# Performance work log

Measured on AMD Instinct MI355X. Metric: run time of the kernel, lower is better.

Reference implementation:

```python
import jax, jax.numpy as jnp
import numpy as np

HEADS = 4
GROUPS = 32
EPS = 1e-5


def setup_inputs() -> dict:
    key = jax.random.key(0)
    ks = jax.random.split(key, 3)
    B, C, H, W = 8, 256, 32, 32
    x = jax.random.normal(ks[0], (B, C, H, W), dtype=jnp.float32)
    gamma = jnp.ones((C,), jnp.float32)
    beta = jnp.zeros((C,), jnp.float32)
    w_qkv = jax.random.normal(ks[1], (3 * C, C), jnp.float32) * (1.0 / np.sqrt(C))
    b_qkv = jnp.zeros((3 * C,), jnp.float32)
    w_proj = jax.random.normal(ks[2], (C, C), jnp.float32) * (1.0 / np.sqrt(C))
    b_proj = jnp.zeros((C,), jnp.float32)
    return {"x": x, "gamma": gamma, "beta": beta, "w_qkv": w_qkv,
            "b_qkv": b_qkv, "w_proj": w_proj, "b_proj": b_proj}


def group_norm(x, gamma, beta):
    B, C, H, W = x.shape
    xg = x.reshape(B, GROUPS, C // GROUPS, H, W)
    mean = xg.mean(axis=(2, 3, 4), keepdims=True)
    var = xg.var(axis=(2, 3, 4), keepdims=True)
    xg = (xg - mean) * jax.lax.rsqrt(var + EPS)
    xn = xg.reshape(B, C, H, W)
    return xn * gamma[None, :, None, None] + beta[None, :, None, None]


def reference(x, gamma, beta, w_qkv, b_qkv, w_proj, b_proj):
    B, C, H, W = x.shape
    hd = C // HEADS  # head dim
    h = group_norm(x, gamma, beta)
    # 1x1 conv == channel matmul: [B,3C,H,W]
    qkv = jnp.einsum('oc,bchw->bohw', w_qkv, h) + b_qkv[None, :, None, None]
    qkv = qkv.reshape(B, 3, HEADS, hd, H * W)
    q, k, v = qkv[:, 0], qkv[:, 1], qkv[:, 2]  # each [B, heads, hd, HW]
    attn = jnp.einsum('bhci,bhcj->bhij', q, k) * (hd ** -0.5)
    attn = jax.nn.softmax(attn, axis=-1)
    out = jnp.einsum('bhij,bhcj->bhci', attn, v).reshape(B, C, H, W)
    proj = jnp.einsum('oc,bchw->bohw', w_proj, out) + b_proj[None, :, None, None]
    return x + proj
```

## Files before the change

kernel.cpp:

```cpp
#include <hip/hip_runtime.h>
#include <hip/hip_bf16.h>

static constexpr int kC = 256;
static constexpr int kN = 1024;

using s16x8 = __attribute__((ext_vector_type(8))) short;
using f32x4 = __attribute__((ext_vector_type(4))) float;
using u32x4 = __attribute__((ext_vector_type(4))) unsigned int;

__device__ inline f32x4 mfma16(s16x8 a, s16x8 b, f32x4 c) {
  return __builtin_amdgcn_mfma_f32_16x16x32_bf16(a, b, c, 0, 0, 0);
}

__device__ inline unsigned short f2bf(float f) {
  unsigned u = __builtin_bit_cast(unsigned, f);
  u = (u + 0x7fffu + ((u >> 16) & 1u)) >> 16;
  return (unsigned short)u;
}

__device__ inline float exp2_fast(float x) {
  float r;
  asm("v_exp_f32 %0, %1" : "=v"(r) : "v"(x));
  return r;
}

__device__ inline unsigned cvt_pk_bf16(float lo, float hi) {
  unsigned r;
  asm("v_cvt_pk_bf16_f32 %0, %1, %2" : "=v"(r) : "v"(lo), "v"(hi));
  return r;
}

static constexpr float kQScale = 0.18033688011112042f;

__global__ __launch_bounds__(256) void prep_kernel(
    const float* __restrict__ x, const float* __restrict__ gamma,
    const float* __restrict__ beta, unsigned short* __restrict__ hTp,
    const float* __restrict__ wq, const float* __restrict__ wp,
    unsigned short* __restrict__ Wqp, unsigned short* __restrict__ Wpp) {
  if (blockIdx.x < 128) {
    const int tid = blockIdx.x * 256 + threadIdx.x;
    const float* src;
    unsigned short* dst;
    if (tid < 24576) {
      const int fragid = tid >> 6, lane = tid & 63;
      const int Mt = fragid >> 3, kt = fragid & 7;
      src = wq + (size_t)(Mt * 16 + (lane & 15)) * 256 + kt * 32 + (lane >> 4) * 8;
      dst = Wqp + (size_t)tid * 8;
    } else {
      const int id = tid - 24576;
      const int fragid = id >> 6, lane = id & 63;
      const int Mt = fragid >> 3, kt = fragid & 7;
      src = wp + (size_t)(Mt * 16 + (lane & 15)) * 256 + kt * 32 + (lane >> 4) * 8;
      dst = Wpp + (size_t)id * 8;
    }
    const float4 f0 = *(const float4*)src;
    const float4 f1 = *(const float4*)(src + 4);
    ushort4 o0, o1;
    o0.x = f2bf(f0.x); o0.y = f2bf(f0.y); o0.z = f2bf(f0.z); o0.w = f2bf(f0.w);
    o1.x = f2bf(f1.x); o1.y = f2bf(f1.y); o1.z = f2bf(f1.z); o1.w = f2bf(f1.w);
    *(ushort4*)dst = o0;
    *(ushort4*)(dst + 4) = o1;
    return;
  }

  const int bg = blockIdx.x - 128;
  const int b = bg & 7, g = bg >> 3;
  const size_t base = ((size_t)b * kC + (size_t)g * 8) * kN;
  const float4* __restrict__ x4 = (const float4*)(x + base);
  const int t = threadIdx.x;

  float vv[8][4];
  float s = 0.f, ss = 0.f;
#pragma unroll
  for (int i = 0; i < 8; ++i) {
    const float4 v = x4[t + 256 * i];
    vv[i][0] = v.x; vv[i][1] = v.y; vv[i][2] = v.z; vv[i][3] = v.w;
    s += v.x + v.y + v.z + v.w;
    ss += v.x * v.x + v.y * v.y + v.z * v.z + v.w * v.w;
  }
#pragma unroll
  for (int off = 32; off > 0; off >>= 1) {
    s += __shfl_xor(s, off);
    ss += __shfl_xor(ss, off);
  }
  __shared__ float rs[4], rss[4];
  const int wave = t >> 6, lane = t & 63;
  if (lane == 0) { rs[wave] = s; rss[wave] = ss; }
  __syncthreads();
  s = rs[0] + rs[1] + rs[2] + rs[3];
  ss = rss[0] + rss[1] + rss[2] + rss[3];
  const float mean = s * (1.f / 8192.f);
  const float var = ss * (1.f / 8192.f) - mean * mean;
  const float rinv = rsqrtf(var + 1e-5f);
  float ga[8], be[8];
#pragma unroll
  for (int i = 0; i < 8; ++i) {
    ga[i] = gamma[g * 8 + i] * rinv;
    be[i] = beta[g * 8 + i] - mean * ga[i];
  }
  const int kt = g >> 2, gq = g & 3;
#pragma unroll
  for (int r = 0; r < 4; ++r) {
    const int pos = 4 * t + r;
    const int nt = pos >> 4, lp = pos & 15;
    unsigned short* dst =
        hTp + ((size_t)((b * 64 + nt) * 8 + kt) * 64 + (gq * 16 + lp)) * 8;
    ushort4 o0, o1;
    o0.x = f2bf(vv[0][r] * ga[0] + be[0]);
    o0.y = f2bf(vv[1][r] * ga[1] + be[1]);
    o0.z = f2bf(vv[2][r] * ga[2] + be[2]);
    o0.w = f2bf(vv[3][r] * ga[3] + be[3]);
    o1.x = f2bf(vv[4][r] * ga[4] + be[4]);
    o1.y = f2bf(vv[5][r] * ga[5] + be[5]);
    o1.z = f2bf(vv[6][r] * ga[6] + be[6]);
    o1.w = f2bf(vv[7][r] * ga[7] + be[7]);
    *(ushort4*)dst = o0;
    *(ushort4*)(dst + 4) = o1;
  }
}

__device__ inline void gload(const s16x8* __restrict__ Af,
                             const s16x8* __restrict__ Bf,
                             int Mt0, int Nt0, int kt, int lane,
                             s16x8 (&a)[4], s16x8 (&bb)[2]) {
#pragma unroll
  for (int mt = 0; mt < 4; ++mt)
    a[mt] = Af[((size_t)(Mt0 + mt) * 8 + kt) * 64 + lane];
#pragma unroll
  for (int nt = 0; nt < 2; ++nt)
    bb[nt] = Bf[((size_t)(Nt0 + nt) * 8 + kt) * 64 + lane];
}

__device__ inline void gmfma(const s16x8 (&a)[4], const s16x8 (&bb)[2],
                             f32x4 (&acc)[4][2], bool swap) {
  if (swap) {
#pragma unroll
    for (int mt = 0; mt < 4; ++mt)
#pragma unroll
      for (int nt = 0; nt < 2; ++nt)
        acc[mt][nt] = mfma16(bb[nt], a[mt], acc[mt][nt]);
  } else {
#pragma unroll
    for (int mt = 0; mt < 4; ++mt)
#pragma unroll
      for (int nt = 0; nt < 2; ++nt)
        acc[mt][nt] = mfma16(a[mt], bb[nt], acc[mt][nt]);
  }
}

__global__ __launch_bounds__(256) void gemm_qkv_kernel(
    const unsigned short* __restrict__ Wp, const float* __restrict__ bias,
    const unsigned short* __restrict__ Bp,
    unsigned short* __restrict__ Qp, unsigned short* __restrict__ Kp,
    unsigned short* __restrict__ Vp) {
  const int bid = blockIdx.x;
  const int swz = (bid & 7) * 96 + (bid >> 3);
  const int b = swz / 96, rr = swz % 96;
  const int mb = rr >> 4, nb = rr & 15;
  const int t = threadIdx.x;
  const int wave = t >> 6, lane = t & 63;
  const int li = lane & 15, grp = lane >> 4;
  const int m0 = mb * 128 + (wave >> 1) * 64;
  const int n0 = nb * 64 + (wave & 1) * 32;
  const bool swap = mb >= 4;
  const int Mt0 = m0 >> 4;
  const int Nt0 = b * 64 + (n0 >> 4);
  const s16x8* __restrict__ Af = (const s16x8*)Wp;
  const s16x8* __restrict__ Bf = (const s16x8*)Bp;

  f32x4 acc[4][2];
#pragma unroll
  for (int mt = 0; mt < 4; ++mt)
#pragma unroll
    for (int nt = 0; nt < 2; ++nt) acc[mt][nt] = f32x4{0.f, 0.f, 0.f, 0.f};

  s16x8 sa[4][4], sb[4][2];
  gload(Af, Bf, Mt0, Nt0, 0, lane, sa[0], sb[0]);
  gload(Af, Bf, Mt0, Nt0, 1, lane, sa[1], sb[1]);
  gload(Af, Bf, Mt0, Nt0, 2, lane, sa[2], sb[2]);
#pragma unroll
  for (int kt = 0; kt < 8; ++kt) {
    if (kt + 3 < 8)
      gload(Af, Bf, Mt0, Nt0, kt + 3, lane, sa[(kt + 3) & 3], sb[(kt + 3) & 3]);
    gmfma(sa[kt & 3], sb[kt & 3], acc, swap);
  }

  if (!swap) {
    unsigned short* __restrict__ Tp = (mb < 2) ? Qp : Kp;
    const float qs = (mb < 2) ? kQScale : 1.0f;
#pragma unroll
    for (int mt = 0; mt < 4; ++mt) {
      const int mbase = m0 + mt * 16;
      const int head = (mbase >> 6) & 3;
      const int bh = b * 4 + head;
      const int c16 = mbase & 63;
      const int ks = c16 >> 5;
      const int grpp = ((c16 >> 3) + (grp >> 1)) & 3;
      const float4 bv = *(const float4*)(bias + mbase + 4 * grp);
#pragma unroll
      for (int nt = 0; nt < 2; ++nt) {
        const int pt = (n0 >> 4) + nt;
        ushort4 o;
        o.x = f2bf((acc[mt][nt][0] + bv.x) * qs);
        o.y = f2bf((acc[mt][nt][1] + bv.y) * qs);
        o.z = f2bf((acc[mt][nt][2] + bv.z) * qs);
        o.w = f2bf((acc[mt][nt][3] + bv.w) * qs);
        *(ushort4*)(Tp + (size_t)bh * 65536 +
                    ((size_t)(pt * 2 + ks) * 64 + grpp * 16 + li) * 8 +
                    (grp & 1) * 4) = o;
      }
    }
  } else {
#pragma unroll
    for (int mt = 0; mt < 4; ++mt) {
      const int mbase = m0 + mt * 16;
      const int head = (mbase >> 6) & 3;
      const int bh = b * 4 + head;
      const int ct = (mbase & 63) >> 4;
      const float bvc = bias[mbase + li];
      const int kvt = n0 >> 5;
#pragma unroll
      for (int nt = 0; nt < 2; ++nt) {
        ushort4 o;
        o.x = f2bf(acc[mt][nt][0] + bvc);
        o.y = f2bf(acc[mt][nt][1] + bvc);
        o.z = f2bf(acc[mt][nt][2] + bvc);
        o.w = f2bf(acc[mt][nt][3] + bvc);
        *(ushort4*)(Vp + (size_t)bh * 65536 +
                    ((size_t)(ct * 32 + kvt) * 64 + grp * 16 + li) * 8 +
                    nt * 4) = o;
      }
    }
  }
}

__global__ __launch_bounds__(512) void attn_proj_kernel(
    const unsigned short* __restrict__ Qp, const unsigned short* __restrict__ Kp,
    const unsigned short* __restrict__ Vp, const unsigned short* __restrict__ Wpp,
    const float* __restrict__ bpj, const float* __restrict__ x,
    float* __restrict__ out) {
  __shared__ __align__(16) unsigned short Ex[2][8][64][8];
  const int bid = blockIdx.x;
  const int swz = (bid & 7) * 32 + (bid >> 3);
  const int b = swz >> 5, qb = swz & 31;
  const int t = threadIdx.x;
  const int w8 = t >> 6, lane = t & 63;
  const int head = w8 & 3, qh = w8 >> 2;
  const int li = lane & 15, grp = lane >> 4;
  const int q0 = qb * 32 + qh * 16;
  const int bh = b * 4 + head;
  const unsigned short* __restrict__ Qb = Qp + (size_t)bh * 65536;
  const unsigned short* __restrict__ Kb = Kp + (size_t)bh * 65536;
  const unsigned short* __restrict__ Vb = Vp + (size_t)bh * 65536;

  s16x8 qf[2];
#pragma unroll
  for (int ks = 0; ks < 2; ++ks)
    qf[ks] = *(const s16x8*)(Qb + (((q0 >> 4) * 2 + ks) * 64 + lane) * 8);

  f32x4 O[4];
#pragma unroll
  for (int ct = 0; ct < 4; ++ct) O[ct] = f32x4{0.f, 0.f, 0.f, 0.f};
  f32x4 lvec = f32x4{0.f, 0.f, 0.f, 0.f};
  float m_run = -1.0e30f;

  auto loadK = [&](int it, s16x8 (&kk)[2][2]) {
#pragma unroll
    for (int mt = 0; mt < 2; ++mt)
#pragma unroll
      for (int ks = 0; ks < 2; ++ks)
        kk[mt][ks] = *(const s16x8*)(
            Kb + ((size_t)((it * 2 + mt) * 2 + ks) * 64 + lane) * 8);
  };
  auto loadV = [&](int it, s16x8 (&vv)[4]) {
#pragma unroll
    for (int ct = 0; ct < 4; ++ct)
      vv[ct] = *(const s16x8*)(Vb + ((size_t)(ct * 32 + it) * 64 + lane) * 8);
  };
  auto qkt = [&](const s16x8 (&kk)[2][2], f32x4 (&s)[2]) {
    __builtin_amdgcn_s_setprio(1);
#pragma unroll
    for (int mt = 0; mt < 2; ++mt) {
      s[mt] = mfma16(kk[mt][0], qf[0], f32x4{0.f, 0.f, 0.f, 0.f});
      s[mt] = mfma16(kk[mt][1], qf[1], s[mt]);
    }
    __builtin_amdgcn_s_setprio(0);
  };
  auto smaxpv = [&](f32x4 (&s)[2], const s16x8 (&vv)[4]) {
    const float A = fmaxf(fmaxf(s[0][0], s[0][1]), s[0][2]);
    const float B = fmaxf(fmaxf(s[0][3], s[1][0]), s[1][1]);
    const float C = fmaxf(fmaxf(s[1][2], s[1][3]), A);
    float pm = fmaxf(B, C);
    pm = fmaxf(pm, __shfl_xor(pm, 16));
    pm = fmaxf(pm, __shfl_xor(pm, 32));
    if (!__all(pm <= m_run + 8.0f)) {
      const float mnew = fmaxf(m_run, pm);
      const float f = exp2_fast(m_run - mnew);
      m_run = mnew;
      lvec *= f;
#pragma unroll
      for (int ct = 0; ct < 4; ++ct) O[ct] *= f;
    }
    f32x4 p[2];
#pragma unroll
    for (int mt = 0; mt < 2; ++mt) {
#pragma unroll
      for (int r = 0; r < 4; ++r) p[mt][r] = exp2_fast(s[mt][r] - m_run);
      lvec += p[mt];
    }
    u32x4 pk;
    pk[0] = cvt_pk_bf16(p[0][0], p[0][1]);
    pk[1] = cvt_pk_bf16(p[0][2], p[0][3]);
    pk[2] = cvt_pk_bf16(p[1][0], p[1][1]);
    pk[3] = cvt_pk_bf16(p[1][2], p[1][3]);
    const s16x8 pf = __builtin_bit_cast(s16x8, pk);
    __builtin_amdgcn_s_setprio(1);
#pragma unroll
    for (int ct = 0; ct < 4; ++ct) O[ct] = mfma16(vv[ct], pf, O[ct]);
    __builtin_amdgcn_s_setprio(0);
  };

  s16x8 K4[4][2][2], V4[4][4];
  loadK(0, K4[0]); loadK(1, K4[1]); loadK(2, K4[2]); loadK(3, K4[3]);
  loadV(0, V4[0]); loadV(1, V4[1]); loadV(2, V4[2]); loadV(3, V4[3]);
  f32x4 sc[2];
  qkt(K4[0], sc);
  loadK(4, K4[0]);

#pragma unroll 1
  for (int g = 0; g < 8; ++g) {
    const int t0 = g * 4;
#pragma unroll
    for (int j = 0; j < 4; ++j) {
      const int tt = t0 + j;
      f32x4 sn[2];
      qkt(K4[(j + 1) & 3], sn);
      loadK(tt + 5, K4[(j + 1) & 3]);
      smaxpv(sc, V4[j]);
      loadV(tt + 4, V4[j]);
      sc[0] = sn[0];
      sc[1] = sn[1];
    }
  }

  float lt = lvec[0] + lvec[1] + lvec[2] + lvec[3];
  lt += __shfl_xor(lt, 16);
  lt += __shfl_xor(lt, 32);
  const float rinv = 1.f / lt;
#pragma unroll
  for (int ct = 0; ct < 4; ++ct) {
    const int ktp = head * 2 + (ct >> 1);
    const int grpp = ((ct & 1) * 2 + (grp >> 1)) & 3;
    ushort4 o;
    o.x = f2bf(O[ct][0] * rinv);
    o.y = f2bf(O[ct][1] * rinv);
    o.z = f2bf(O[ct][2] * rinv);
    o.w = f2bf(O[ct][3] * rinv);
    *(ushort4*)&Ex[qh][ktp][grpp * 16 + li][(grp & 1) * 4] = o;
  }
  __syncthreads();

  {
    const int Mt0 = w8 * 2;
    const s16x8* __restrict__ Af = (const s16x8*)Wpp;
    f32x4 acc[2][2];
#pragma unroll
    for (int mt = 0; mt < 2; ++mt)
#pragma unroll
      for (int nt = 0; nt < 2; ++nt) acc[mt][nt] = f32x4{0.f, 0.f, 0.f, 0.f};

    s16x8 pa[3][2];
    auto loadA = [&](int kt, s16x8 (&a)[2]) {
#pragma unroll
      for (int mt = 0; mt < 2; ++mt)
        a[mt] = Af[((size_t)(Mt0 + mt) * 8 + kt) * 64 + lane];
    };
    loadA(0, pa[0]);
    loadA(1, pa[1]);
#pragma unroll
    for (int kt = 0; kt < 8; ++kt) {
      if (kt + 2 < 8) loadA(kt + 2, pa[(kt + 2) % 3]);
      s16x8 bb[2];
#pragma unroll
      for (int nt = 0; nt < 2; ++nt)
        bb[nt] = *(const s16x8*)&Ex[nt][kt][lane][0];
#pragma unroll
      for (int mt = 0; mt < 2; ++mt)
#pragma unroll
        for (int nt = 0; nt < 2; ++nt)
          acc[mt][nt] = mfma16(pa[kt % 3][mt], bb[nt], acc[mt][nt]);
    }

#pragma unroll
    for (int mt = 0; mt < 2; ++mt) {
      const int mbase = w8 * 32 + mt * 16 + 4 * grp;
      const float4 bv = *(const float4*)(bpj + mbase);
      const float bvr[4] = {bv.x, bv.y, bv.z, bv.w};
#pragma unroll
      for (int nt = 0; nt < 2; ++nt) {
        const int pos = qb * 32 + nt * 16 + li;
#pragma unroll
        for (int r2 = 0; r2 < 4; ++r2) {
          const size_t ob = ((size_t)(b * 256 + mbase + r2)) * 1024 + pos;
          out[ob] = acc[mt][nt][r2] + bvr[r2] + x[ob];
        }
      }
    }
  }
}

extern "C" void kernel_launch(void* const* d_in, const int* in_sizes, int n_in,
                              void* d_out, int out_size, void* d_ws, size_t ws_size,
                              hipStream_t stream) {
  const float* x      = (const float*)d_in[0];
  const float* gamma  = (const float*)d_in[1];
  const float* beta   = (const float*)d_in[2];
  const float* w_qkv  = (const float*)d_in[3];
  const float* b_qkv  = (const float*)d_in[4];
  const float* w_proj = (const float*)d_in[5];
  const float* b_proj = (const float*)d_in[6];
  float* out = (float*)d_out;

  unsigned short* ws = (unsigned short*)d_ws;
  unsigned short* Wqp  = ws;
  unsigned short* Wpp  = Wqp + 196608;
  unsigned short* hTp  = Wpp + 65536;
  unsigned short* Qp   = hTp + 2097152;
  unsigned short* Kp   = Qp + 2097152;
  unsigned short* Vp   = Kp + 2097152;

  hipLaunchKernelGGL(prep_kernel, dim3(384), dim3(256), 0, stream,
                     x, gamma, beta, hTp, w_qkv, w_proj, Wqp, Wpp);
  hipLaunchKernelGGL(gemm_qkv_kernel, dim3(768), dim3(256), 0, stream,
                     Wqp, b_qkv, hTp, Qp, Kp, Vp);
  hipLaunchKernelGGL(attn_proj_kernel, dim3(256), dim3(512), 0, stream,
                     Qp, Kp, Vp, Wpp, b_proj, x, out);
}
```

Measured before the change: 42.58 us.

## Split attention and projection, stage K/V tiles in LDS shared across query waves

The fused attention+projection kernel is split into two kernels. In the new attention kernel, each 256-thread block handles one (batch, head) with 64 queries over four waves. K/V tiles are loaded once per block into double-buffered LDS with global_load_lds and shared by all waves, instead of every wave streaming its own register copies. The output projection becomes a separate GEMM kernel that reads attention output from a new workspace buffer. This adds a kernel launch, a global round trip for the attention output, and a per-iteration __syncthreads that replaces the deep register prefetch pipeline.

Measured after the change: 51.06 us. +19.9%, slower.

```diff
diff --git a/kernel.cpp b/kernel.cpp
--- a/kernel.cpp
+++ b/kernel.cpp
@@ -28,6 +28,12 @@
   unsigned r;
   asm("v_cvt_pk_bf16_f32 %0, %1, %2" : "=v"(r) : "v"(lo), "v"(hi));
   return r;
+}
+
+__device__ inline void gl_lds16(const void* g, void* l) {
+  typedef __attribute__((address_space(1))) const unsigned int GU;
+  typedef __attribute__((address_space(3))) unsigned int LU;
+  __builtin_amdgcn_global_load_lds((GU*)g, (LU*)l, 16, 0, 0);
 }
 
 static constexpr float kQScale = 0.18033688011112042f;
@@ -234,21 +240,20 @@
   }
 }
 
-__global__ __launch_bounds__(512) void attn_proj_kernel(
+__global__ __launch_bounds__(256) void attn_kernel(
     const unsigned short* __restrict__ Qp, const unsigned short* __restrict__ Kp,
-    const unsigned short* __restrict__ Vp, const unsigned short* __restrict__ Wpp,
-    const float* __restrict__ bpj, const float* __restrict__ x,
-    float* __restrict__ out) {
-  __shared__ __align__(16) unsigned short Ex[2][8][64][8];
+    const unsigned short* __restrict__ Vp, unsigned short* __restrict__ aoTp) {
+  __shared__ __align__(16) unsigned short Kl[2][2048];
+  __shared__ __align__(16) unsigned short Vl[2][2048];
   const int bid = blockIdx.x;
-  const int swz = (bid & 7) * 32 + (bid >> 3);
-  const int b = swz >> 5, qb = swz & 31;
+  const int xcd = bid & 7, idx = bid >> 3;
+  const int bh = xcd * 4 + (idx & 3);
+  const int qb = idx >> 2;
+  const int b = bh >> 2, head = bh & 3;
   const int t = threadIdx.x;
-  const int w8 = t >> 6, lane = t & 63;
-  const int head = w8 & 3, qh = w8 >> 2;
+  const int wave = t >> 6, lane = t & 63;
   const int li = lane & 15, grp = lane >> 4;
-  const int q0 = qb * 32 + qh * 16;
-  const int bh = b * 4 + head;
+  const int q0 = qb * 64 + wave * 16;
   const unsigned short* __restrict__ Qb = Qp + (size_t)bh * 65536;
   const unsigned short* __restrict__ Kb = Kp + (size_t)bh * 65536;
   const unsigned short* __restrict__ Vb = Vp + (size_t)bh * 65536;
@@ -264,20 +269,27 @@
   f32x4 lvec = f32x4{0.f, 0.f, 0.f, 0.f};
   float m_run = -1.0e30f;
 
-  auto loadK = [&](int it, s16x8 (&kk)[2][2]) {
+  auto stage = [&](int it, int nb) {
+    const unsigned short* ksrc = Kb + ((size_t)(it * 4 + wave) * 512 + lane * 8);
+    gl_lds16(ksrc, &Kl[nb][wave * 512]);
+    const unsigned short* vsrc = Vb + ((size_t)(wave * 32 + it) * 512 + lane * 8);
+    gl_lds16(vsrc, &Vl[nb][wave * 512]);
+  };
+
+  stage(0, 0);
+  __syncthreads();
+
+  int cb = 0;
+#pragma unroll 1
+  for (int it = 0; it < 32; ++it) {
+    if (it < 31) stage(it + 1, cb ^ 1);
+    s16x8 kk[2][2];
 #pragma unroll
     for (int mt = 0; mt < 2; ++mt)
 #pragma unroll
       for (int ks = 0; ks < 2; ++ks)
-        kk[mt][ks] = *(const s16x8*)(
-            Kb + ((size_t)((it * 2 + mt) * 2 + ks) * 64 + lane) * 8);
-  };
-  auto loadV = [&](int it, s16x8 (&vv)[4]) {
-#pragma unroll
-    for (int ct = 0; ct < 4; ++ct)
-      vv[ct] = *(const s16x8*)(Vb + ((size_t)(ct * 32 + it) * 64 + lane) * 8);
-  };
-  auto qkt = [&](const s16x8 (&kk)[2][2], f32x4 (&s)[2]) {
+        kk[mt][ks] = *(const s16x8*)&Kl[cb][(mt * 2 + ks) * 512 + lane * 8];
+    f32x4 s[2];
     __builtin_amdgcn_s_setprio(1);
 #pragma unroll
     for (int mt = 0; mt < 2; ++mt) {
@@ -285,8 +297,6 @@
       s[mt] = mfma16(kk[mt][1], qf[1], s[mt]);
     }
     __builtin_amdgcn_s_setprio(0);
-  };
-  auto smaxpv = [&](f32x4 (&s)[2], const s16x8 (&vv)[4]) {
     const float A = fmaxf(fmaxf(s[0][0], s[0][1]), s[0][2]);
     const float B = fmaxf(fmaxf(s[0][3], s[1][0]), s[1][1]);
     const float C = fmaxf(fmaxf(s[1][2], s[1][3]), A);
@@ -314,33 +324,16 @@
     pk[2] = cvt_pk_bf16(p[1][0], p[1][1]);
     pk[3] = cvt_pk_bf16(p[1][2], p[1][3]);
     const s16x8 pf = __builtin_bit_cast(s16x8, pk);
+    s16x8 vv[4];
+#pragma unroll
+    for (int ct = 0; ct < 4; ++ct)
+      vv[ct] = *(const s16x8*)&Vl[cb][ct * 512 + lane * 8];
     __builtin_amdgcn_s_setprio(1);
 #pragma unroll
     for (int ct = 0; ct < 4; ++ct) O[ct] = mfma16(vv[ct], pf, O[ct]);
     __builtin_amdgcn_s_setprio(0);
-  };
-
-  s16x8 K4[4][2][2], V4[4][4];
-  loadK(0, K4[0]); loadK(1, K4[1]); loadK(2, K4[2]); loadK(3, K4[3]);
-  loadV(0, V4[0]); loadV(1, V4[1]); loadV(2, V4[2]); loadV(3, V4[3]);
-  f32x4 sc[2];
-  qkt(K4[0], sc);
-  loadK(4, K4[0]);
-
-#pragma unroll 1
-  for (int g = 0; g < 8; ++g) {
-    const int t0 = g * 4;
-#pragma unroll
-    for (int j = 0; j < 4; ++j) {
-      const int tt = t0 + j;
-      f32x4 sn[2];
-      qkt(K4[(j + 1) & 3], sn);
-      loadK(tt + 5, K4[(j + 1) & 3]);
-      smaxpv(sc, V4[j]);
-      loadV(tt + 4, V4[j]);
-      sc[0] = sn[0];
-      sc[1] = sn[1];
-    }
+    __syncthreads();
+    cb ^= 1;
   }
 
   float lt = lvec[0] + lvec[1] + lvec[2] + lvec[3];
@@ -356,54 +349,59 @@
     o.y = f2bf(O[ct][1] * rinv);
     o.z = f2bf(O[ct][2] * rinv);
     o.w = f2bf(O[ct][3] * rinv);
-    *(ushort4*)&Ex[qh][ktp][grpp * 16 + li][(grp & 1) * 4] = o;
-  }
-  __syncthreads();
-
-  {
-    const int Mt0 = w8 * 2;
-    const s16x8* __restrict__ Af = (const s16x8*)Wpp;
-    f32x4 acc[2][2];
-#pragma unroll
-    for (int mt = 0; mt < 2; ++mt)
-#pragma unroll
-      for (int nt = 0; nt < 2; ++nt) acc[mt][nt] = f32x4{0.f, 0.f, 0.f, 0.f};
-
-    s16x8 pa[3][2];
-    auto loadA = [&](int kt, s16x8 (&a)[2]) {
-#pragma unroll
-      for (int mt = 0; mt < 2; ++mt)
-        a[mt] = Af[((size_t)(Mt0 + mt) * 8 + kt) * 64 + lane];
-    };
-    loadA(0, pa[0]);
-    loadA(1, pa[1]);
-#pragma unroll
-    for (int kt = 0; kt < 8; ++kt) {
-      if (kt + 2 < 8) loadA(kt + 2, pa[(kt + 2) % 3]);
-      s16x8 bb[2];
-#pragma unroll
-      for (int nt = 0; nt < 2; ++nt)
-        bb[nt] = *(const s16x8*)&Ex[nt][kt][lane][0];
-#pragma unroll
-      for (int mt = 0; mt < 2; ++mt)
-#pragma unroll
-        for (int nt = 0; nt < 2; ++nt)
-          acc[mt][nt] = mfma16(pa[kt % 3][mt], bb[nt], acc[mt][nt]);
-    }
-
-#pragma unroll
-    for (int mt = 0; mt < 2; ++mt) {
-      const int mbase = w8 * 32 + mt * 16 + 4 * grp;
-      const float4 bv = *(const float4*)(bpj + mbase);
-      const float bvr[4] = {bv.x, bv.y, bv.z, bv.w};
-#pragma unroll
-      for (int nt = 0; nt < 2; ++nt) {
-        const int pos = qb * 32 + nt * 16 + li;
-#pragma unroll
-        for (int r2 = 0; r2 < 4; ++r2) {
-          const size_t ob = ((size_t)(b * 256 + mbase + r2)) * 1024 + pos;
-          out[ob] = acc[mt][nt][r2] + bvr[r2] + x[ob];
-        }
+    *(ushort4*)(aoTp +
+                ((size_t)((b * 64 + (q0 >> 4)) * 8 + ktp) * 64 + grpp * 16 + li) * 8 +
+                (grp & 1) * 4) = o;
+  }
+}
+
+__global__ __launch_bounds__(256) void gemm_proj_kernel(
+    const unsigned short* __restrict__ Wpp, const float* __restrict__ bias,
+    const unsigned short* __restrict__ aoTp, const float* __restrict__ res,
+    float* __restrict__ outp) {
+  const int bid = blockIdx.x;
+  const int swz = (bid & 7) * 32 + (bid >> 3);
+  const int b = swz >> 5, rr = swz & 31;
+  const int mb = rr >> 4, nb = rr & 15;
+  const int t = threadIdx.x;
+  const int wave = t >> 6, lane = t & 63;
+  const int li = lane & 15, grp = lane >> 4;
+  const int m0 = mb * 128 + (wave >> 1) * 64;
+  const int n0 = nb * 64 + (wave & 1) * 32;
+  const int Mt0 = m0 >> 4;
+  const int Nt0 = b * 64 + (n0 >> 4);
+  const s16x8* __restrict__ Af = (const s16x8*)Wpp;
+  const s16x8* __restrict__ Bf = (const s16x8*)aoTp;
+
+  f32x4 acc[4][2];
+#pragma unroll
+  for (int mt = 0; mt < 4; ++mt)
+#pragma unroll
+    for (int nt = 0; nt < 2; ++nt) acc[mt][nt] = f32x4{0.f, 0.f, 0.f, 0.f};
+
+  s16x8 sa[4][4], sb[4][2];
+  gload(Af, Bf, Mt0, Nt0, 0, lane, sa[0], sb[0]);
+  gload(Af, Bf, Mt0, Nt0, 1, lane, sa[1], sb[1]);
+  gload(Af, Bf, Mt0, Nt0, 2, lane, sa[2], sb[2]);
+#pragma unroll
+  for (int kt = 0; kt < 8; ++kt) {
+    if (kt + 3 < 8)
+      gload(Af, Bf, Mt0, Nt0, kt + 3, lane, sa[(kt + 3) & 3], sb[(kt + 3) & 3]);
+    gmfma(sa[kt & 3], sb[kt & 3], acc, false);
+  }
+
+#pragma unroll
+  for (int mt = 0; mt < 4; ++mt) {
+    const int mbase = m0 + mt * 16 + 4 * grp;
+    const float4 bv = *(const float4*)(bias + mbase);
+    const float bvr[4] = {bv.x, bv.y, bv.z, bv.w};
+#pragma unroll
+    for (int nt = 0; nt < 2; ++nt) {
+      const int pos = n0 + nt * 16 + li;
+#pragma unroll
+      for (int r = 0; r < 4; ++r) {
+        const size_t ob = ((size_t)(b * 256 + mbase + r)) * 1024 + pos;
+        outp[ob] = acc[mt][nt][r] + bvr[r] + res[ob];
       }
     }
   }
@@ -428,11 +426,14 @@
   unsigned short* Qp   = hTp + 2097152;
   unsigned short* Kp   = Qp + 2097152;
   unsigned short* Vp   = Kp + 2097152;
+  unsigned short* aoTp = Vp + 2097152;
 
   hipLaunchKernelGGL(prep_kernel, dim3(384), dim3(256), 0, stream,
                      x, gamma, beta, hTp, w_qkv, w_proj, Wqp, Wpp);
   hipLaunchKernelGGL(gemm_qkv_kernel, dim3(768), dim3(256), 0, stream,
                      Wqp, b_qkv, hTp, Qp, Kp, Vp);
-  hipLaunchKernelGGL(attn_proj_kernel, dim3(256), dim3(512), 0, stream,
-                     Qp, Kp, Vp, Wpp, b_proj, x, out);
-}
+  hipLaunchKernelGGL(attn_kernel, dim3(512), dim3(256), 0, stream,
+                     Qp, Kp, Vp, aoTp);
+  hipLaunchKernelGGL(gemm_proj_kernel, dim3(256), dim3(256), 0, stream,
+                     Wpp, b_proj, aoTp, x, out);
+}
```

## Split attention keys across waves and merge partial softmax states in LDS

Applied to the files above, without the earlier changes.

The attention kernel now gives each block 16 query positions instead of 32 and doubles the grid to 512 blocks. The two wave halves each process half of the key sequence, and the partial O, max and sum are combined through shared memory, split-K flash-decoding style. The deep register prefetch ring for K/V is dropped in favour of a simple loop with launch_bounds occupancy hint 4, aiming for more parallelism and occupancy on 256 CUs. The risks are the loss of explicit load/compute overlap, an extra LDS merge and sync, and half the reuse of the projection weights per block.

Measured after the change: 42.48 us. Within noise of the previous version (-0.2%).

```diff
diff --git a/kernel.cpp b/kernel.cpp
--- a/kernel.cpp
+++ b/kernel.cpp
@@ -234,20 +234,21 @@
   }
 }
 
-__global__ __launch_bounds__(512) void attn_proj_kernel(
+__global__ __launch_bounds__(512, 4) void attn_proj_kernel(
     const unsigned short* __restrict__ Qp, const unsigned short* __restrict__ Kp,
     const unsigned short* __restrict__ Vp, const unsigned short* __restrict__ Wpp,
     const float* __restrict__ bpj, const float* __restrict__ x,
     float* __restrict__ out) {
-  __shared__ __align__(16) unsigned short Ex[2][8][64][8];
+  __shared__ __align__(16) float Ml[4][64][18];
+  __shared__ __align__(16) unsigned short Ex[8][64][8];
   const int bid = blockIdx.x;
-  const int swz = (bid & 7) * 32 + (bid >> 3);
-  const int b = swz >> 5, qb = swz & 31;
+  const int b = bid & 7;
+  const int pb = bid >> 3;
+  const int q0 = pb * 16;
   const int t = threadIdx.x;
   const int w8 = t >> 6, lane = t & 63;
-  const int head = w8 & 3, qh = w8 >> 2;
+  const int head = w8 & 3, khalf = w8 >> 2;
   const int li = lane & 15, grp = lane >> 4;
-  const int q0 = qb * 32 + qh * 16;
   const int bh = b * 4 + head;
   const unsigned short* __restrict__ Qb = Qp + (size_t)bh * 65536;
   const unsigned short* __restrict__ Kb = Kp + (size_t)bh * 65536;
@@ -256,28 +257,30 @@
   s16x8 qf[2];
 #pragma unroll
   for (int ks = 0; ks < 2; ++ks)
-    qf[ks] = *(const s16x8*)(Qb + (((q0 >> 4) * 2 + ks) * 64 + lane) * 8);
+    qf[ks] = *(const s16x8*)(Qb + ((pb * 2 + ks) * 64 + lane) * 8);
 
   f32x4 O[4];
 #pragma unroll
   for (int ct = 0; ct < 4; ++ct) O[ct] = f32x4{0.f, 0.f, 0.f, 0.f};
   f32x4 lvec = f32x4{0.f, 0.f, 0.f, 0.f};
   float m_run = -1.0e30f;
-
-  auto loadK = [&](int it, s16x8 (&kk)[2][2]) {
+  const int kbase = khalf * 16;
+
+#pragma unroll 1
+  for (int i2 = 0; i2 < 16; ++i2) {
+    const int it = kbase + i2;
+    s16x8 kk[2][2];
 #pragma unroll
     for (int mt = 0; mt < 2; ++mt)
 #pragma unroll
       for (int ks = 0; ks < 2; ++ks)
         kk[mt][ks] = *(const s16x8*)(
             Kb + ((size_t)((it * 2 + mt) * 2 + ks) * 64 + lane) * 8);
-  };
-  auto loadV = [&](int it, s16x8 (&vv)[4]) {
+    s16x8 vv[4];
 #pragma unroll
     for (int ct = 0; ct < 4; ++ct)
       vv[ct] = *(const s16x8*)(Vb + ((size_t)(ct * 32 + it) * 64 + lane) * 8);
-  };
-  auto qkt = [&](const s16x8 (&kk)[2][2], f32x4 (&s)[2]) {
+    f32x4 s[2];
     __builtin_amdgcn_s_setprio(1);
 #pragma unroll
     for (int mt = 0; mt < 2; ++mt) {
@@ -285,8 +288,6 @@
       s[mt] = mfma16(kk[mt][1], qf[1], s[mt]);
     }
     __builtin_amdgcn_s_setprio(0);
-  };
-  auto smaxpv = [&](f32x4 (&s)[2], const s16x8 (&vv)[4]) {
     const float A = fmaxf(fmaxf(s[0][0], s[0][1]), s[0][2]);
     const float B = fmaxf(fmaxf(s[0][3], s[1][0]), s[1][1]);
     const float C = fmaxf(fmaxf(s[1][2], s[1][3]), A);
@@ -318,56 +319,49 @@
 #pragma unroll
     for (int ct = 0; ct < 4; ++ct) O[ct] = mfma16(vv[ct], pf, O[ct]);
     __builtin_amdgcn_s_setprio(0);
-  };
-
-  s16x8 K4[4][2][2], V4[4][4];
-  loadK(0, K4[0]); loadK(1, K4[1]); loadK(2, K4[2]); loadK(3, K4[3]);
-  loadV(0, V4[0]); loadV(1, V4[1]); loadV(2, V4[2]); loadV(3, V4[3]);
-  f32x4 sc[2];
-  qkt(K4[0], sc);
-  loadK(4, K4[0]);
-
-#pragma unroll 1
-  for (int g = 0; g < 8; ++g) {
-    const int t0 = g * 4;
-#pragma unroll
-    for (int j = 0; j < 4; ++j) {
-      const int tt = t0 + j;
-      f32x4 sn[2];
-      qkt(K4[(j + 1) & 3], sn);
-      loadK(tt + 5, K4[(j + 1) & 3]);
-      smaxpv(sc, V4[j]);
-      loadV(tt + 4, V4[j]);
-      sc[0] = sn[0];
-      sc[1] = sn[1];
-    }
   }
 
   float lt = lvec[0] + lvec[1] + lvec[2] + lvec[3];
   lt += __shfl_xor(lt, 16);
   lt += __shfl_xor(lt, 32);
-  const float rinv = 1.f / lt;
-#pragma unroll
-  for (int ct = 0; ct < 4; ++ct) {
-    const int ktp = head * 2 + (ct >> 1);
-    const int grpp = ((ct & 1) * 2 + (grp >> 1)) & 3;
-    ushort4 o;
-    o.x = f2bf(O[ct][0] * rinv);
-    o.y = f2bf(O[ct][1] * rinv);
-    o.z = f2bf(O[ct][2] * rinv);
-    o.w = f2bf(O[ct][3] * rinv);
-    *(ushort4*)&Ex[qh][ktp][grpp * 16 + li][(grp & 1) * 4] = o;
+
+  if (khalf == 1) {
+    float* dst = &Ml[head][lane][0];
+#pragma unroll
+    for (int ct = 0; ct < 4; ++ct) *(f32x4*)(dst + ct * 4) = O[ct];
+    dst[16] = m_run;
+    dst[17] = lt;
+  }
+  __syncthreads();
+  if (khalf == 0) {
+    const float* src = &Ml[head][lane][0];
+    const float mB = src[16], lB = src[17];
+    const float mS = fmaxf(m_run, mB);
+    const float fA = exp2_fast(m_run - mS);
+    const float fB = exp2_fast(mB - mS);
+    const float rinv = 1.f / (lt * fA + lB * fB);
+    const float a = fA * rinv, bs = fB * rinv;
+#pragma unroll
+    for (int ct = 0; ct < 4; ++ct) {
+      const f32x4 ob = *(const f32x4*)(src + ct * 4);
+      ushort4 o;
+      o.x = f2bf(O[ct][0] * a + ob[0] * bs);
+      o.y = f2bf(O[ct][1] * a + ob[1] * bs);
+      o.z = f2bf(O[ct][2] * a + ob[2] * bs);
+      o.w = f2bf(O[ct][3] * a + ob[3] * bs);
+      const int ktp = head * 2 + (ct >> 1);
+      const int grpp = ((ct & 1) * 2 + (grp >> 1)) & 3;
+      *(ushort4*)&Ex[ktp][grpp * 16 + li][(grp & 1) * 4] = o;
+    }
   }
   __syncthreads();
 
   {
     const int Mt0 = w8 * 2;
     const s16x8* __restrict__ Af = (const s16x8*)Wpp;
-    f32x4 acc[2][2];
-#pragma unroll
-    for (int mt = 0; mt < 2; ++mt)
-#pragma unroll
-      for (int nt = 0; nt < 2; ++nt) acc[mt][nt] = f32x4{0.f, 0.f, 0.f, 0.f};
+    f32x4 acc[2];
+    acc[0] = f32x4{0.f, 0.f, 0.f, 0.f};
+    acc[1] = f32x4{0.f, 0.f, 0.f, 0.f};
 
     s16x8 pa[3][2];
     auto loadA = [&](int kt, s16x8 (&a)[2]) {
@@ -380,15 +374,10 @@
 #pragma unroll
     for (int kt = 0; kt < 8; ++kt) {
       if (kt + 2 < 8) loadA(kt + 2, pa[(kt + 2) % 3]);
-      s16x8 bb[2];
-#pragma unroll
-      for (int nt = 0; nt < 2; ++nt)
-        bb[nt] = *(const s16x8*)&Ex[nt][kt][lane][0];
+      const s16x8 bb = *(const s16x8*)&Ex[kt][lane][0];
 #pragma unroll
       for (int mt = 0; mt < 2; ++mt)
-#pragma unroll
-        for (int nt = 0; nt < 2; ++nt)
-          acc[mt][nt] = mfma16(pa[kt % 3][mt], bb[nt], acc[mt][nt]);
+        acc[mt] = mfma16(pa[kt % 3][mt], bb, acc[mt]);
     }
 
 #pragma unroll
@@ -396,14 +385,11 @@
       const int mbase = w8 * 32 + mt * 16 + 4 * grp;
       const float4 bv = *(const float4*)(bpj + mbase);
       const float bvr[4] = {bv.x, bv.y, bv.z, bv.w};
-#pragma unroll
-      for (int nt = 0; nt < 2; ++nt) {
-        const int pos = qb * 32 + nt * 16 + li;
-#pragma unroll
-        for (int r2 = 0; r2 < 4; ++r2) {
-          const size_t ob = ((size_t)(b * 256 + mbase + r2)) * 1024 + pos;
-          out[ob] = acc[mt][nt][r2] + bvr[r2] + x[ob];
-        }
+      const int pos = q0 + li;
+#pragma unroll
+      for (int r2 = 0; r2 < 4; ++r2) {
+        const size_t ob = ((size_t)(b * 256 + mbase + r2)) * 1024 + pos;
+        out[ob] = acc[mt][r2] + bvr[r2] + x[ob];
       }
     }
   }
@@ -433,6 +419,6 @@
                      x, gamma, beta, hTp, w_qkv, w_proj, Wqp, Wpp);
   hipLaunchKernelGGL(gemm_qkv_kernel, dim3(768), dim3(256), 0, stream,
                      Wqp, b_qkv, hTp, Qp, Kp, Vp);
-  hipLaunchKernelGGL(attn_proj_kernel, dim3(256), dim3(512), 0, stream,
+  hipLaunchKernelGGL(attn_proj_kernel, dim3(512), dim3(512), 0, stream,
                      Qp, Kp, Vp, Wpp, b_proj, x, out);
 }
```

## Split KV range across wave pairs with split-K softmax merge in LDS

Applied to the files above, without the earlier changes.

Each wave now handles both 16-query halves of a 32-query block for one head, but only half of the key/value sequence. Partial outputs, running max and sum are merged through shared memory before the projection stage. This halves K/V loads per wave, because each loaded K/V tile serves two query tiles, and shortens the serial loop. In exchange it adds a merge step, an extra barrier and about 37KB more shared memory. The block-to-batch mapping and swizzle also change, and the deep four-stage prefetch is replaced by double buffering.

Result: faster. 36.06 us, median of 2 (-15.3%).

```diff
diff --git a/kernel.cpp b/kernel.cpp
--- a/kernel.cpp
+++ b/kernel.cpp
@@ -239,30 +239,37 @@
     const unsigned short* __restrict__ Vp, const unsigned short* __restrict__ Wpp,
     const float* __restrict__ bpj, const float* __restrict__ x,
     float* __restrict__ out) {
+  __shared__ __align__(16) float Ml[4][2][64][18];
   __shared__ __align__(16) unsigned short Ex[2][8][64][8];
   const int bid = blockIdx.x;
-  const int swz = (bid & 7) * 32 + (bid >> 3);
-  const int b = swz >> 5, qb = swz & 31;
+  const int b = bid & 7;
+  const int pb = bid >> 3;
   const int t = threadIdx.x;
   const int w8 = t >> 6, lane = t & 63;
-  const int head = w8 & 3, qh = w8 >> 2;
+  const int head = w8 & 3, khalf = w8 >> 2;
   const int li = lane & 15, grp = lane >> 4;
-  const int q0 = qb * 32 + qh * 16;
   const int bh = b * 4 + head;
   const unsigned short* __restrict__ Qb = Qp + (size_t)bh * 65536;
   const unsigned short* __restrict__ Kb = Kp + (size_t)bh * 65536;
   const unsigned short* __restrict__ Vb = Vp + (size_t)bh * 65536;
 
-  s16x8 qf[2];
-#pragma unroll
-  for (int ks = 0; ks < 2; ++ks)
-    qf[ks] = *(const s16x8*)(Qb + (((q0 >> 4) * 2 + ks) * 64 + lane) * 8);
-
-  f32x4 O[4];
-#pragma unroll
-  for (int ct = 0; ct < 4; ++ct) O[ct] = f32x4{0.f, 0.f, 0.f, 0.f};
-  f32x4 lvec = f32x4{0.f, 0.f, 0.f, 0.f};
-  float m_run = -1.0e30f;
+  s16x8 qf[2][2];
+#pragma unroll
+  for (int qh = 0; qh < 2; ++qh)
+#pragma unroll
+    for (int ks = 0; ks < 2; ++ks)
+      qf[qh][ks] = *(const s16x8*)(Qb + (((pb * 2 + qh) * 2 + ks) * 64 + lane) * 8);
+
+  f32x4 O[2][4];
+  f32x4 lvec[2];
+  float m_run[2] = {-1.0e30f, -1.0e30f};
+#pragma unroll
+  for (int qh = 0; qh < 2; ++qh) {
+    lvec[qh] = f32x4{0.f, 0.f, 0.f, 0.f};
+#pragma unroll
+    for (int ct = 0; ct < 4; ++ct) O[qh][ct] = f32x4{0.f, 0.f, 0.f, 0.f};
+  }
+  const int kbase = khalf * 16;
 
   auto loadK = [&](int it, s16x8 (&kk)[2][2]) {
 #pragma unroll
@@ -277,86 +284,112 @@
     for (int ct = 0; ct < 4; ++ct)
       vv[ct] = *(const s16x8*)(Vb + ((size_t)(ct * 32 + it) * 64 + lane) * 8);
   };
-  auto qkt = [&](const s16x8 (&kk)[2][2], f32x4 (&s)[2]) {
+
+  auto body = [&](const s16x8 (&kk)[2][2], const s16x8 (&vv)[4]) {
+    f32x4 s[2][2];
     __builtin_amdgcn_s_setprio(1);
 #pragma unroll
-    for (int mt = 0; mt < 2; ++mt) {
-      s[mt] = mfma16(kk[mt][0], qf[0], f32x4{0.f, 0.f, 0.f, 0.f});
-      s[mt] = mfma16(kk[mt][1], qf[1], s[mt]);
-    }
+    for (int qh = 0; qh < 2; ++qh)
+#pragma unroll
+      for (int mt = 0; mt < 2; ++mt) {
+        s[qh][mt] = mfma16(kk[mt][0], qf[qh][0], f32x4{0.f, 0.f, 0.f, 0.f});
+        s[qh][mt] = mfma16(kk[mt][1], qf[qh][1], s[qh][mt]);
+      }
     __builtin_amdgcn_s_setprio(0);
+#pragma unroll
+    for (int qh = 0; qh < 2; ++qh) {
+      const float A = fmaxf(fmaxf(s[qh][0][0], s[qh][0][1]), s[qh][0][2]);
+      const float B = fmaxf(fmaxf(s[qh][0][3], s[qh][1][0]), s[qh][1][1]);
+      const float C = fmaxf(fmaxf(s[qh][1][2], s[qh][1][3]), A);
+      float pm = fmaxf(B, C);
+      pm = fmaxf(pm, __shfl_xor(pm, 16));
+      pm = fmaxf(pm, __shfl_xor(pm, 32));
+      if (!__all(pm <= m_run[qh] + 8.0f)) {
+        const float mnew = fmaxf(m_run[qh], pm);
+        const float f = exp2_fast(m_run[qh] - mnew);
+        m_run[qh] = mnew;
+        lvec[qh] *= f;
+#pragma unroll
+        for (int ct = 0; ct < 4; ++ct) O[qh][ct] *= f;
+      }
+      f32x4 p[2];
+#pragma unroll
+      for (int mt = 0; mt < 2; ++mt) {
+#pragma unroll
+        for (int r = 0; r < 4; ++r) p[mt][r] = exp2_fast(s[qh][mt][r] - m_run[qh]);
+        lvec[qh] += p[mt];
+      }
+      u32x4 pk;
+      pk[0] = cvt_pk_bf16(p[0][0], p[0][1]);
+      pk[1] = cvt_pk_bf16(p[0][2], p[0][3]);
+      pk[2] = cvt_pk_bf16(p[1][0], p[1][1]);
+      pk[3] = cvt_pk_bf16(p[1][2], p[1][3]);
+      const s16x8 pf = __builtin_bit_cast(s16x8, pk);
+      __builtin_amdgcn_s_setprio(1);
+#pragma unroll
+      for (int ct = 0; ct < 4; ++ct) O[qh][ct] = mfma16(vv[ct], pf, O[qh][ct]);
+      __builtin_amdgcn_s_setprio(0);
+    }
   };
-  auto smaxpv = [&](f32x4 (&s)[2], const s16x8 (&vv)[4]) {
-    const float A = fmaxf(fmaxf(s[0][0], s[0][1]), s[0][2]);
-    const float B = fmaxf(fmaxf(s[0][3], s[1][0]), s[1][1]);
-    const float C = fmaxf(fmaxf(s[1][2], s[1][3]), A);
-    float pm = fmaxf(B, C);
-    pm = fmaxf(pm, __shfl_xor(pm, 16));
-    pm = fmaxf(pm, __shfl_xor(pm, 32));
-    if (!__all(pm <= m_run + 8.0f)) {
-      const float mnew = fmaxf(m_run, pm);
-      const float f = exp2_fast(m_run - mnew);
-      m_run = mnew;
-      lvec *= f;
-#pragma unroll
-      for (int ct = 0; ct < 4; ++ct) O[ct] *= f;
-    }
-    f32x4 p[2];
-#pragma unroll
-    for (int mt = 0; mt < 2; ++mt) {
-#pragma unroll
-      for (int r = 0; r < 4; ++r) p[mt][r] = exp2_fast(s[mt][r] - m_run);
-      lvec += p[mt];
-    }
-    u32x4 pk;
-    pk[0] = cvt_pk_bf16(p[0][0], p[0][1]);
-    pk[1] = cvt_pk_bf16(p[0][2], p[0][3]);
-    pk[2] = cvt_pk_bf16(p[1][0], p[1][1]);
-    pk[3] = cvt_pk_bf16(p[1][2], p[1][3]);
-    const s16x8 pf = __builtin_bit_cast(s16x8, pk);
-    __builtin_amdgcn_s_setprio(1);
-#pragma unroll
-    for (int ct = 0; ct < 4; ++ct) O[ct] = mfma16(vv[ct], pf, O[ct]);
-    __builtin_amdgcn_s_setprio(0);
-  };
-
-  s16x8 K4[4][2][2], V4[4][4];
-  loadK(0, K4[0]); loadK(1, K4[1]); loadK(2, K4[2]); loadK(3, K4[3]);
-  loadV(0, V4[0]); loadV(1, V4[1]); loadV(2, V4[2]); loadV(3, V4[3]);
-  f32x4 sc[2];
-  qkt(K4[0], sc);
-  loadK(4, K4[0]);
-
+
+  {
+    s16x8 k0[2][2], k1[2][2], v0[4], v1[4];
+    loadK(kbase, k0);
+    loadV(kbase, v0);
 #pragma unroll 1
-  for (int g = 0; g < 8; ++g) {
-    const int t0 = g * 4;
-#pragma unroll
-    for (int j = 0; j < 4; ++j) {
-      const int tt = t0 + j;
-      f32x4 sn[2];
-      qkt(K4[(j + 1) & 3], sn);
-      loadK(tt + 5, K4[(j + 1) & 3]);
-      smaxpv(sc, V4[j]);
-      loadV(tt + 4, V4[j]);
-      sc[0] = sn[0];
-      sc[1] = sn[1];
-    }
-  }
-
-  float lt = lvec[0] + lvec[1] + lvec[2] + lvec[3];
-  lt += __shfl_xor(lt, 16);
-  lt += __shfl_xor(lt, 32);
-  const float rinv = 1.f / lt;
-#pragma unroll
-  for (int ct = 0; ct < 4; ++ct) {
-    const int ktp = head * 2 + (ct >> 1);
-    const int grpp = ((ct & 1) * 2 + (grp >> 1)) & 3;
-    ushort4 o;
-    o.x = f2bf(O[ct][0] * rinv);
-    o.y = f2bf(O[ct][1] * rinv);
-    o.z = f2bf(O[ct][2] * rinv);
-    o.w = f2bf(O[ct][3] * rinv);
-    *(ushort4*)&Ex[qh][ktp][grpp * 16 + li][(grp & 1) * 4] = o;
+    for (int h2 = 0; h2 < 8; ++h2) {
+      const int it = kbase + 2 * h2;
+      loadK(it + 1, k1);
+      loadV(it + 1, v1);
+      body(k0, v0);
+      loadK(it + 2, k0);
+      loadV(it + 2, v0);
+      body(k1, v1);
+    }
+  }
+
+  float lt[2];
+#pragma unroll
+  for (int qh = 0; qh < 2; ++qh) {
+    lt[qh] = lvec[qh][0] + lvec[qh][1] + lvec[qh][2] + lvec[qh][3];
+    lt[qh] += __shfl_xor(lt[qh], 16);
+    lt[qh] += __shfl_xor(lt[qh], 32);
+  }
+
+  if (khalf == 1) {
+#pragma unroll
+    for (int qh = 0; qh < 2; ++qh) {
+      float* dst = &Ml[head][qh][lane][0];
+#pragma unroll
+      for (int ct = 0; ct < 4; ++ct) *(f32x4*)(dst + ct * 4) = O[qh][ct];
+      dst[16] = m_run[qh];
+      dst[17] = lt[qh];
+    }
+  }
+  __syncthreads();
+  if (khalf == 0) {
+#pragma unroll
+    for (int qh = 0; qh < 2; ++qh) {
+      const float* src = &Ml[head][qh][lane][0];
+      const float mB = src[16], lB = src[17];
+      const float mS = fmaxf(m_run[qh], mB);
+      const float fA = exp2_fast(m_run[qh] - mS);
+      const float fB = exp2_fast(mB - mS);
+      const float rinv = 1.f / (lt[qh] * fA + lB * fB);
+      const float a = fA * rinv, bs = fB * rinv;
+#pragma unroll
+      for (int ct = 0; ct < 4; ++ct) {
+        const f32x4 ob = *(const f32x4*)(src + ct * 4);
+        ushort4 o;
+        o.x = f2bf(O[qh][ct][0] * a + ob[0] * bs);
+        o.y = f2bf(O[qh][ct][1] * a + ob[1] * bs);
+        o.z = f2bf(O[qh][ct][2] * a + ob[2] * bs);
+        o.w = f2bf(O[qh][ct][3] * a + ob[3] * bs);
+        const int ktp = head * 2 + (ct >> 1);
+        const int grpp = ((ct & 1) * 2 + (grp >> 1)) & 3;
+        *(ushort4*)&Ex[qh][ktp][grpp * 16 + li][(grp & 1) * 4] = o;
+      }
+    }
   }
   __syncthreads();
 
@@ -398,7 +431,7 @@
       const float bvr[4] = {bv.x, bv.y, bv.z, bv.w};
 #pragma unroll
       for (int nt = 0; nt < 2; ++nt) {
-        const int pos = qb * 32 + nt * 16 + li;
+        const int pos = pb * 32 + nt * 16 + li;
 #pragma unroll
         for (int r2 = 0; r2 < 4; ++r2) {
           const size_t ob = ((size_t)(b * 256 + mbase + r2)) * 1024 + pos;
```
